# Optimization experiments

Hardware: AMD Instinct MI355X
Metric: run time of the kernel (lower is better)

Reference implementation:

```python
import jax, jax.numpy as jnp
import numpy as np

H = W = 512
MAX_ID = 15          # instance ids 1..15 (0 = background)
N_SIGMA = 1
FG_WEIGHT = 1.0
W_INST, W_VAR, W_SEED = 1.0, 10.0, 1.0


def make_xym(h, w):
    # channel 0 varies along width (x), channel 1 along height (y), like the torch buffer
    xs = jnp.linspace(0.0, 1.0, 512)
    xm = jnp.broadcast_to(xs[None, None, :], (1, 512, 512))
    ym = jnp.broadcast_to(xs[None, :, None], (1, 512, 512))
    xym = jnp.concatenate([xm, ym], axis=0)
    return xym[:, :h, :w]


def lovasz_hinge_flat(logits, labels):
    # logits, labels: flat [P]; labels in {0,1} float
    signs = 2.0 * labels - 1.0
    errors = 1.0 - logits * signs
    perm = jnp.argsort(-errors)                 # descending
    errors_sorted = errors[perm]
    gt_sorted = labels[perm]
    gts = jnp.sum(gt_sorted)
    intersection = gts - jnp.cumsum(gt_sorted)
    union = gts + jnp.cumsum(1.0 - gt_sorted)
    jaccard = 1.0 - intersection / union
    jaccard = jnp.concatenate([jaccard[:1], jaccard[1:] - jaccard[:-1]])
    return jnp.sum(jax.nn.relu(errors_sorted) * jaccard)


def _per_image(pred_b, inst_b, lab_b, xym):
    spatial_emb = jnp.tanh(pred_b[0:2]) + xym          # (2,H,W)
    sigma = pred_b[2]                                  # (H,W), n_sigma=1
    seed_map = jax.nn.sigmoid(pred_b[3])               # (H,W)

    bg = (lab_b == 0)
    seed_bg = jnp.sum(jnp.where(bg, seed_map ** 2, 0.0))

    def per_inst(iid):
        m = (inst_b == iid).astype(pred_b.dtype)       # (H,W)
        cnt = jnp.sum(m)
        present = cnt > 0
        cnt_s = jnp.maximum(cnt, 1.0)
        # to_center=True: center from coordinate map
        center = jnp.sum(xym * m[None], axis=(1, 2)) / cnt_s            # (2,)
        sig_mean = jnp.sum(sigma * m) / cnt_s
        var_l = jnp.sum((sigma - jax.lax.stop_gradient(sig_mean)) ** 2 * m) / cnt_s
        s = jnp.exp(sig_mean * 10.0)
        d2 = jnp.sum((spatial_emb - center[:, None, None]) ** 2, axis=0)  # (H,W)
        dist = jnp.exp(-d2 * s)
        inst_l = lovasz_hinge_flat(dist.reshape(-1) * 2.0 - 1.0, m.reshape(-1))
        seed_l = jnp.sum((seed_map - jax.lax.stop_gradient(dist)) ** 2 * m)
        intra_l = 1.0 - jnp.sum(dist * m) / cnt_s
        return present, var_l, inst_l, seed_l, intra_l

    ids = jnp.arange(1, MAX_ID + 1)
    present, var_l, inst_l, seed_l, intra_l = jax.vmap(per_inst)(ids)
    pf = present.astype(pred_b.dtype)
    obj = jnp.sum(pf)
    obj_s = jnp.maximum(obj, 1.0)
    instance_loss = jnp.sum(inst_l * pf) / obj_s
    var_loss = jnp.sum(var_l * pf) / obj_s
    intra_loss = jnp.sum(intra_l * pf)          # NOT divided by obj_count (as in source)
    seed_loss = (seed_bg + FG_WEIGHT * jnp.sum(seed_l * pf)) / (H * W)
    return W_INST * instance_loss + W_VAR * var_loss + W_SEED * seed_loss + 5.0 * intra_loss


def setup_inputs() -> dict:
    key = jax.random.key(0)
    k1, k2, k3 = jax.random.split(key, 3)
    prediction = jax.random.normal(k1, (4, 4, H, W), dtype=jnp.float32)
    instances = jax.random.randint(k2, (4, H, W), 0, MAX_ID + 1, dtype=jnp.int32)
    labels = jax.random.randint(k3, (4, H, W), 0, 2, dtype=jnp.int32)
    return {"prediction": prediction, "instances": instances, "labels": labels}


def reference(prediction, instances, labels):
    xym = make_xym(prediction.shape[2], prediction.shape[3])
    per_b = jax.vmap(_per_image, in_axes=(0, 0, 0, None))(prediction, instances, labels, xym)
    return jnp.mean(per_b)
```

## Files before the change

### kernel.cpp

```cpp
#include <hip/hip_runtime.h>

#define HW     262144
#define NB     4
#define NID    15
#define KB     256
#define CHUNKS 128
#define PXC    (HW / CHUNKS)

#define WS_TICKET 0
#define WS_GACC   4
#define WS_SBGR   24
#define WS_PART   64
#define PART_STR  1024
#define WS_FACC   65600
#define WS_HIST   90432
#define HIST_U32  (NB * CHUNKS * NID * KB)
#define WS_EMBX   (WS_HIST + HIST_U32)
#define MAP_SZ    (NB * HW)
#define WS_EMBY   (WS_EMBX + MAP_SZ)
#define WS_SEEDM  (WS_EMBY + MAP_SZ)
#define WS_TOTAL  (WS_SEEDM + MAP_SZ)

__device__ __forceinline__ float rcp_fast(float x) { return __builtin_amdgcn_rcpf(x); }
__device__ __forceinline__ float fast_tanh(float x) {
    return 1.0f - 2.0f * rcp_fast(__expf(2.0f * x) + 1.0f);
}
__device__ __forceinline__ float fast_sigmoid(float x) {
    return rcp_fast(1.0f + __expf(-x));
}
__device__ __forceinline__ float atomic_read(float* p) { return atomicAdd(p, 0.0f); }

__global__ __launch_bounds__(256) void prepKernel(const float* __restrict__ pred,
                                                  const int* __restrict__ inst,
                                                  const int* __restrict__ lab,
                                                  float* __restrict__ ws) {
    __shared__ float s_acc[16][68];
    const int b   = blockIdx.y;
    const int tid = threadIdx.x;
    for (int j = tid; j < 16 * 68; j += 256) ((float*)s_acc)[j] = 0.f;
    __syncthreads();

    const int grp = tid >> 4;
    const int ib = b * HW;
    const float* p0 = pred + (((size_t)(b * 4 + 0)) << 18);
    const float* p1 = pred + (((size_t)(b * 4 + 1)) << 18);
    const float* p2 = pred + (((size_t)(b * 4 + 2)) << 18);
    const float* p3 = pred + (((size_t)(b * 4 + 3)) << 18);
    float* embx  = ws + WS_EMBX + ib;
    float* emby  = ws + WS_EMBY + ib;
    float* seedm = ws + WS_SEEDM + ib;
    const float inv511 = 1.0f / 511.0f;

    const int p = blockIdx.x * 1024 + tid * 4;
    const int4   i4 = *(const int4*)(inst + ib + p);
    const int4   l4 = *(const int4*)(lab + ib + p);
    const float4 a4 = *(const float4*)(p0 + p);
    const float4 b4 = *(const float4*)(p1 + p);
    const float4 g4 = *(const float4*)(p2 + p);
    const float4 t4 = *(const float4*)(p3 + p);
    const float xs0 = (float)(p & 511) * inv511;
    const float ys  = (float)(p >> 9) * inv511;

    float4 ex, ey, sd;
    ex.x = fast_tanh(a4.x) + xs0;
    ex.y = fast_tanh(a4.y) + xs0 + inv511;
    ex.z = fast_tanh(a4.z) + xs0 + 2.f * inv511;
    ex.w = fast_tanh(a4.w) + xs0 + 3.f * inv511;
    ey.x = fast_tanh(b4.x) + ys;
    ey.y = fast_tanh(b4.y) + ys;
    ey.z = fast_tanh(b4.z) + ys;
    ey.w = fast_tanh(b4.w) + ys;
    sd.x = fast_sigmoid(t4.x);
    sd.y = fast_sigmoid(t4.y);
    sd.z = fast_sigmoid(t4.z);
    sd.w = fast_sigmoid(t4.w);
    *(float4*)(embx + p)  = ex;
    *(float4*)(emby + p)  = ey;
    *(float4*)(seedm + p) = sd;

    float sbg = 0.f;
    sbg += (l4.x == 0) ? sd.x * sd.x : 0.f;
    sbg += (l4.y == 0) ? sd.y * sd.y : 0.f;
    sbg += (l4.z == 0) ? sd.z * sd.z : 0.f;
    sbg += (l4.w == 0) ? sd.w * sd.w : 0.f;

#define ACC_PX(IID, XS, SG)                                   \
    if ((IID) > 0) {                                          \
        float* a = &s_acc[grp][((IID) - 1) * 4];              \
        atomicAdd(a + 0, 1.f);                                \
        atomicAdd(a + 1, (XS));                               \
        atomicAdd(a + 2, ys);                                 \
        atomicAdd(a + 3, (SG));                               \
    }
    ACC_PX(i4.x, xs0, g4.x)
    ACC_PX(i4.y, xs0 + inv511, g4.y)
    ACC_PX(i4.z, xs0 + 2.f * inv511, g4.z)
    ACC_PX(i4.w, xs0 + 3.f * inv511, g4.w)
#undef ACC_PX

#pragma unroll
    for (int m = 32; m; m >>= 1) sbg += __shfl_xor(sbg, m, 64);
    if ((tid & 63) == 0) atomicAdd(&s_acc[grp][60], sbg);
    __syncthreads();

    if (tid < 61) {
        float tot = 0.f;
#pragma unroll
        for (int q = 0; q < 16; ++q) tot += s_acc[q][tid];
        ws[WS_PART + tid * PART_STR + b * 256 + blockIdx.x] = tot;
    }
    if (blockIdx.x == 0 && b == 0) {
        if (tid < 20)       ws[WS_GACC + tid] = 0.f;
        else if (tid == 20) ((unsigned*)ws)[WS_TICKET] = 0u;
    }
}

#define HCOPY_STRIDE (NID * KB + 1)
__global__ __launch_bounds__(256) void histKernel(const float* __restrict__ pred,
                                                  const int* __restrict__ inst,
                                                  float* __restrict__ ws) {
    __shared__ unsigned s_hist[4 * HCOPY_STRIDE];
    __shared__ float4   s_stat4[NID];
    __shared__ float    s_facc[8][48];
    __shared__ float    s_comp[61];

    const int b     = blockIdx.y;
    const int chunk = blockIdx.x;
    const int tid   = threadIdx.x;
    const int wv = tid >> 6, lane = tid & 63;

    for (int c = wv; c < 61; c += 4) {
        const float* pp = ws + WS_PART + c * PART_STR + b * 256;
        float v = pp[lane] + pp[lane + 64] + pp[lane + 128] + pp[lane + 192];
#pragma unroll
        for (int m = 32; m; m >>= 1) v += __shfl_xor(v, m, 64);
        if (lane == 0) s_comp[c] = v;
    }
    for (int j = tid; j < 4 * HCOPY_STRIDE; j += 256) s_hist[j] = 0u;
    for (int j = tid; j < 8 * 48; j += 256) ((float*)s_facc)[j] = 0.f;
    __syncthreads();

    if (tid < NID) {
        float cnt = s_comp[tid * 4 + 0];
        float ic = rcp_fast(fmaxf(cnt, 1.f));
        float sigm = s_comp[tid * 4 + 3] * ic;
        s_stat4[tid] = make_float4(s_comp[tid * 4 + 1] * ic, s_comp[tid * 4 + 2] * ic,
                                   sigm, __expf(10.f * sigm));
    }
    if (chunk == 0 && tid == 16) ws[WS_SBGR + b] = s_comp[60];
    __syncthreads();

    float csx[NID], csy[NID], css[NID];
#pragma unroll
    for (int i = 0; i < NID; ++i) {
        float4 v = s_stat4[i];
        csx[i] = v.x; csy[i] = v.y; css[i] = v.w;
    }

    unsigned* myhist = &s_hist[((tid >> 4) & 3) * HCOPY_STRIDE];
    float* myfacc = s_facc[(tid >> 3) & 7];
    const int ib = b * HW;
    const float* sig   = pred + (((size_t)(b * 4 + 2)) << 18);
    const float* embx  = ws + WS_EMBX + ib;
    const float* emby  = ws + WS_EMBY + ib;
    const float* seedm = ws + WS_SEEDM + ib;

    auto doPx = [&](float exv, float eyv, float sdv, float gv, int iid) {
#pragma unroll
        for (int i = 0; i < NID; ++i) {
            float dx = exv - csx[i], dy = eyv - csy[i];
            float dist = __expf(-(dx * dx + dy * dy) * css[i]);
            float u1 = dist * (float)KB;
            bool m = (iid == i + 1);
            float bf = m ? ((float)KB - u1) : u1;
            int bk = min((int)bf, KB - 1);
            atomicAdd(&myhist[i * KB + bk], m ? 1u : 0x10000u);
        }
        if (iid > 0) {
            float4 st = s_stat4[iid - 1];
            float dx = exv - st.x, dy = eyv - st.y;
            float dist = __expf(-(dx * dx + dy * dy) * st.w);
            float dsg = gv - st.z;
            float e2 = sdv - dist;
            float* fa = &myfacc[(iid - 1) * 3];
            atomicAdd(fa + 0, dsg * dsg);
            atomicAdd(fa + 1, e2 * e2);
            atomicAdd(fa + 2, dist);
        }
    };

#pragma unroll
    for (int u = 0; u < 2; ++u) {
        const int p = chunk * PXC + u * 1024 + tid * 4;
        const int4   i4 = *(const int4*)(inst + ib + p);
        const float4 exq = *(const float4*)(embx + p);
        const float4 eyq = *(const float4*)(emby + p);
        const float4 sdq = *(const float4*)(seedm + p);
        const float4 gq  = *(const float4*)(sig + p);
        doPx(exq.x, eyq.x, sdq.x, gq.x, i4.x);
        doPx(exq.y, eyq.y, sdq.y, gq.y, i4.y);
        doPx(exq.z, eyq.z, sdq.z, gq.z, i4.z);
        doPx(exq.w, eyq.w, sdq.w, gq.w, i4.w);
    }
    __syncthreads();

    unsigned* dst = (unsigned*)(ws + WS_HIST) + (size_t)(b * CHUNKS + chunk) * (NID * KB);
    for (int j = tid; j < NID * KB; j += 256) {
        dst[j] = s_hist[j] + s_hist[HCOPY_STRIDE + j] +
                 s_hist[2 * HCOPY_STRIDE + j] + s_hist[3 * HCOPY_STRIDE + j];
    }
    if (tid < 45) {
        float tot = 0.f;
#pragma unroll
        for (int q = 0; q < 8; ++q) tot += s_facc[q][tid];
        ws[WS_FACC + (size_t)(b * CHUNKS + chunk) * 48 + tid] = tot;
    }
}

__global__ __launch_bounds__(256) void lovaszKernel(float* __restrict__ ws,
                                                    float* __restrict__ out) {
    __shared__ unsigned s_pf[4][KB];
    __shared__ unsigned s_pb[4][KB];
    __shared__ float s4[4];
    __shared__ float s_f[4][3];
    const int t = blockIdx.x;
    const int b = t / NID, i = t % NID;
    const int tid = threadIdx.x, wv = tid >> 6, lane = tid & 63;

    {
        float g = ws[WS_PART + (i * 4) * PART_STR + b * 256 + tid];
#pragma unroll
        for (int m = 32; m; m >>= 1) g += __shfl_xor(g, m, 64);
        if (lane == 0) s4[wv] = g;
    }
    {
        float f0 = 0.f, f1 = 0.f, f2 = 0.f;
        if (tid < CHUNKS) {
            const float* fb = ws + WS_FACC + (size_t)(b * CHUNKS + tid) * 48 + i * 3;
            f0 = fb[0]; f1 = fb[1]; f2 = fb[2];
        }
#pragma unroll
        for (int m = 32; m; m >>= 1) {
            f0 += __shfl_xor(f0, m, 64);
            f1 += __shfl_xor(f1, m, 64);
            f2 += __shfl_xor(f2, m, 64);
        }
        if (lane == 0) { s_f[wv][0] = f0; s_f[wv][1] = f1; s_f[wv][2] = f2; }
    }
    __syncthreads();
    const float G = s4[0] + s4[1] + s4[2] + s4[3];

    if (G > 0.f) {
        unsigned af0 = 0, af1 = 0, af2 = 0, af3 = 0;
        unsigned ab0 = 0, ab1 = 0, ab2 = 0, ab3 = 0;
        const unsigned* histU = (const unsigned*)(ws + WS_HIST);
        for (int k = 0; k < 32; ++k) {
            const int c = wv * 32 + k;
            const unsigned* hb = histU + ((size_t)(b * CHUNKS + c) * NID + i) * KB + lane * 4;
            uint4 q = *(const uint4*)hb;
            af0 += q.x & 0xffffu; ab0 += q.x >> 16;
            af1 += q.y & 0xffffu; ab1 += q.y >> 16;
            af2 += q.z & 0xffffu; ab2 += q.z >> 16;
            af3 += q.w & 0xffffu; ab3 += q.w >> 16;
        }
        s_pf[wv][lane * 4 + 0] = af0; s_pb[wv][lane * 4 + 0] = ab0;
        s_pf[wv][lane * 4 + 1] = af1; s_pb[wv][lane * 4 + 1] = ab1;
        s_pf[wv][lane * 4 + 2] = af2; s_pb[wv][lane * 4 + 2] = ab2;
        s_pf[wv][lane * 4 + 3] = af3; s_pb[wv][lane * 4 + 3] = ab3;
    }
    __syncthreads();

    float sum = 0.f;
    if (wv == 0 && G > 0.f) {
        float fgs[4], bgs[4];
#pragma unroll
        for (int q = 0; q < 4; ++q) {
            int k = lane * 4 + q;
            fgs[q] = (float)(s_pf[0][k] + s_pf[1][k] + s_pf[2][k] + s_pf[3][k]);
            bgs[q] = (float)(s_pb[0][k] + s_pb[1][k] + s_pb[2][k] + s_pb[3][k]);
        }
        float Fl = fgs[0] + fgs[1] + fgs[2] + fgs[3];
        float Bl = bgs[0] + bgs[1] + bgs[2] + bgs[3];
        float Fs = Fl, Bs = Bl;
#pragma unroll
        for (int d = 1; d < 64; d <<= 1) {
            float fu = __shfl_down(Fs, d, 64);
            float bu = __shfl_down(Bs, d, 64);
            if (lane + d < 64) { Fs += fu; Bs += bu; }
        }
        float F = Fs - Fl, B = Bs - Bl;
        float Jprev = 1.f - (G - F) * rcp_fast(G + B);
        const float ew = 2.f / (float)KB;
#pragma unroll
        for (int q = 3; q >= 0; --q) {
            F += fgs[q]; B += bgs[q];
            float J = 1.f - (G - F) * rcp_fast(G + B);
            float ek = ((float)(lane * 4 + q) + 0.5f) * ew;
            sum += ek * (J - Jprev);
            Jprev = J;
        }
#pragma unroll
        for (int m = 32; m; m >>= 1) sum += __shfl_xor(sum, m, 64);
    }

    if (tid == 0 && G > 0.f) {
        float ic = rcp_fast(fmaxf(G, 1.f));
        float F0 = s_f[0][0] + s_f[1][0] + s_f[2][0] + s_f[3][0];
        float F1 = s_f[0][1] + s_f[1][1] + s_f[2][1] + s_f[3][1];
        float F2 = s_f[0][2] + s_f[1][2] + s_f[2][2] + s_f[3][2];
        float* ga = ws + WS_GACC + b * 5;
        atomicAdd(ga + 0, 1.f);
        atomicAdd(ga + 1, sum);
        atomicAdd(ga + 2, F0 * ic);
        atomicAdd(ga + 3, 1.f - F2 * ic);
        atomicAdd(ga + 4, F1);
    }
    __threadfence();
    if (tid == 0) {
        unsigned tk = atomicAdd((unsigned*)ws + WS_TICKET, 1u);
        if (tk == 59u) {
            float total = 0.f;
            for (int bb = 0; bb < NB; ++bb) {
                float* ga = ws + WS_GACC + bb * 5;
                float obj   = atomic_read(ga + 0);
                float instl = atomic_read(ga + 1);
                float varl  = atomic_read(ga + 2);
                float intral= atomic_read(ga + 3);
                float seedl = atomic_read(ga + 4);
                float sbg   = ws[WS_SBGR + bb];
                float objs  = fmaxf(obj, 1.f);
                total += instl / objs
                       + 10.f * (varl / objs)
                       + (sbg + seedl) / (float)HW
                       + 5.f * intral;
            }
            out[0] = total * 0.25f;
        }
    }
}

extern "C" void kernel_launch(void* const* d_in, const int* in_sizes, int n_in,
                              void* d_out, int out_size, void* d_ws, size_t ws_size,
                              hipStream_t stream) {
    const float* pred = (const float*)d_in[0];
    const int*   inst = (const int*)d_in[1];
    const int*   lab  = (const int*)d_in[2];
    float* ws  = (float*)d_ws;
    float* out = (float*)d_out;

    prepKernel<<<dim3(256, NB), 256, 0, stream>>>(pred, inst, lab, ws);
    histKernel<<<dim3(CHUNKS, NB), 256, 0, stream>>>(pred, inst, ws);
    lovaszKernel<<<60, 256, 0, stream>>>(ws, out);
}
```

Measured before the change: 83.63 us.

## Add stat-reduction kernel, halve histogram bins, reuse matched distance, use exp2

Moves the per-instance centre/sigma reduction out of every histogram block into a small dedicated kernel that writes precomputed stats, so each hist block no longer re-reduces 61 partial arrays. Halves the Lovasz histogram to 128 bins with twice as many chunks, which shrinks per-block shared memory and the per-chunk copy-out, and doubles the number of hist blocks. Folds the bin scale into an exp2 exponent and reuses the matched instance's distance instead of recomputing it. The coarser bins change the Lovasz approximation accuracy, and the extra kernel launch adds some overhead.

```diff
diff --git a/kernel.cpp b/kernel.cpp
--- a/kernel.cpp
+++ b/kernel.cpp
@@ -3,17 +3,19 @@
 #define HW     262144
 #define NB     4
 #define NID    15
-#define KB     256
-#define CHUNKS 128
+#define KB     128
+#define CHUNKS 256
 #define PXC    (HW / CHUNKS)
 
 #define WS_TICKET 0
 #define WS_GACC   4
-#define WS_SBGR   24
-#define WS_PART   64
+#define WS_SBG    24
+#define WS_CNT    28
+#define WS_STAT4  96
+#define WS_PART   512
 #define PART_STR  1024
-#define WS_FACC   65600
-#define WS_HIST   90432
+#define WS_FACC   62976
+#define WS_HIST   112128
 #define HIST_U32  (NB * CHUNKS * NID * KB)
 #define WS_EMBX   (WS_HIST + HIST_U32)
 #define MAP_SZ    (NB * HW)
@@ -21,12 +23,19 @@
 #define WS_SEEDM  (WS_EMBY + MAP_SZ)
 #define WS_TOTAL  (WS_SEEDM + MAP_SZ)
 
+#if __has_builtin(__builtin_amdgcn_exp2f)
+#define EXP2(x) __builtin_amdgcn_exp2f(x)
+#else
+#define EXP2(x) exp2f(x)
+#endif
+#define LOG2E 1.44269504f
+
 __device__ __forceinline__ float rcp_fast(float x) { return __builtin_amdgcn_rcpf(x); }
 __device__ __forceinline__ float fast_tanh(float x) {
-    return 1.0f - 2.0f * rcp_fast(__expf(2.0f * x) + 1.0f);
+    return 1.0f - 2.0f * rcp_fast(EXP2(2.0f * LOG2E * x) + 1.0f);
 }
 __device__ __forceinline__ float fast_sigmoid(float x) {
-    return rcp_fast(1.0f + __expf(-x));
+    return rcp_fast(1.0f + EXP2(-LOG2E * x));
 }
 __device__ __forceinline__ float atomic_read(float* p) { return atomicAdd(p, 0.0f); }
 
@@ -109,9 +118,35 @@
         for (int q = 0; q < 16; ++q) tot += s_acc[q][tid];
         ws[WS_PART + tid * PART_STR + b * 256 + blockIdx.x] = tot;
     }
-    if (blockIdx.x == 0 && b == 0) {
-        if (tid < 20)       ws[WS_GACC + tid] = 0.f;
-        else if (tid == 20) ((unsigned*)ws)[WS_TICKET] = 0u;
+}
+
+__global__ __launch_bounds__(256) void statRedKernel(float* __restrict__ ws) {
+    __shared__ float s_red[61];
+    const int b = blockIdx.x;
+    const int tid = threadIdx.x, wv = tid >> 6, lane = tid & 63;
+
+    for (int c = wv; c < 61; c += 4) {
+        const float* pp = ws + WS_PART + c * PART_STR + b * 256;
+        float v = pp[lane] + pp[lane + 64] + pp[lane + 128] + pp[lane + 192];
+#pragma unroll
+        for (int m = 32; m; m >>= 1) v += __shfl_xor(v, m, 64);
+        if (lane == 0) s_red[c] = v;
+    }
+    __syncthreads();
+
+    if (tid < NID) {
+        float cnt = s_red[tid * 4 + 0];
+        float ic = rcp_fast(fmaxf(cnt, 1.f));
+        float sigm = s_red[tid * 4 + 3] * ic;
+        float sp = EXP2(10.f * LOG2E * sigm) * LOG2E;
+        *(float4*)(ws + WS_STAT4 + (b * NID + tid) * 4) =
+            make_float4(s_red[tid * 4 + 1] * ic, s_red[tid * 4 + 2] * ic, sigm, sp);
+        ws[WS_CNT + b * NID + tid] = cnt;
+    }
+    if (tid == 15) ws[WS_SBG + b] = s_red[60];
+    if (b == 0) {
+        if (tid >= 32 && tid < 52) ws[WS_GACC + tid - 32] = 0.f;
+        if (tid == 52)             ((unsigned*)ws)[WS_TICKET] = 0u;
     }
 }
 
@@ -122,39 +157,21 @@
     __shared__ unsigned s_hist[4 * HCOPY_STRIDE];
     __shared__ float4   s_stat4[NID];
     __shared__ float    s_facc[8][48];
-    __shared__ float    s_comp[61];
 
     const int b     = blockIdx.y;
     const int chunk = blockIdx.x;
     const int tid   = threadIdx.x;
-    const int wv = tid >> 6, lane = tid & 63;
-
-    for (int c = wv; c < 61; c += 4) {
-        const float* pp = ws + WS_PART + c * PART_STR + b * 256;
-        float v = pp[lane] + pp[lane + 64] + pp[lane + 128] + pp[lane + 192];
-#pragma unroll
-        for (int m = 32; m; m >>= 1) v += __shfl_xor(v, m, 64);
-        if (lane == 0) s_comp[c] = v;
-    }
+
+    if (tid < NID) s_stat4[tid] = *(const float4*)(ws + WS_STAT4 + (b * NID + tid) * 4);
     for (int j = tid; j < 4 * HCOPY_STRIDE; j += 256) s_hist[j] = 0u;
     for (int j = tid; j < 8 * 48; j += 256) ((float*)s_facc)[j] = 0.f;
     __syncthreads();
 
-    if (tid < NID) {
-        float cnt = s_comp[tid * 4 + 0];
-        float ic = rcp_fast(fmaxf(cnt, 1.f));
-        float sigm = s_comp[tid * 4 + 3] * ic;
-        s_stat4[tid] = make_float4(s_comp[tid * 4 + 1] * ic, s_comp[tid * 4 + 2] * ic,
-                                   sigm, __expf(10.f * sigm));
-    }
-    if (chunk == 0 && tid == 16) ws[WS_SBGR + b] = s_comp[60];
-    __syncthreads();
-
-    float csx[NID], csy[NID], css[NID];
+    float csx[NID], csy[NID], csp[NID];
 #pragma unroll
     for (int i = 0; i < NID; ++i) {
         float4 v = s_stat4[i];
-        csx[i] = v.x; csy[i] = v.y; css[i] = v.w;
+        csx[i] = v.x; csy[i] = v.y; csp[i] = v.w;
     }
 
     unsigned* myhist = &s_hist[((tid >> 4) & 3) * HCOPY_STRIDE];
@@ -166,21 +183,22 @@
     const float* seedm = ws + WS_SEEDM + ib;
 
     auto doPx = [&](float exv, float eyv, float sdv, float gv, int iid) {
+        float u1m = 0.f;
 #pragma unroll
         for (int i = 0; i < NID; ++i) {
             float dx = exv - csx[i], dy = eyv - csy[i];
-            float dist = __expf(-(dx * dx + dy * dy) * css[i]);
-            float u1 = dist * (float)KB;
+            float d2 = dx * dx + dy * dy;
+            float u1 = EXP2(7.0f - d2 * csp[i]);
             bool m = (iid == i + 1);
+            if (m) u1m = u1;
             float bf = m ? ((float)KB - u1) : u1;
             int bk = min((int)bf, KB - 1);
             atomicAdd(&myhist[i * KB + bk], m ? 1u : 0x10000u);
         }
         if (iid > 0) {
-            float4 st = s_stat4[iid - 1];
-            float dx = exv - st.x, dy = eyv - st.y;
-            float dist = __expf(-(dx * dx + dy * dy) * st.w);
-            float dsg = gv - st.z;
+            float dist = u1m * (1.f / (float)KB);
+            float sigm = s_stat4[iid - 1].z;
+            float dsg = gv - sigm;
             float e2 = sdv - dist;
             float* fa = &myfacc[(iid - 1) * 3];
             atomicAdd(fa + 0, dsg * dsg);
@@ -189,19 +207,16 @@
         }
     };
 
-#pragma unroll
-    for (int u = 0; u < 2; ++u) {
-        const int p = chunk * PXC + u * 1024 + tid * 4;
-        const int4   i4 = *(const int4*)(inst + ib + p);
-        const float4 exq = *(const float4*)(embx + p);
-        const float4 eyq = *(const float4*)(emby + p);
-        const float4 sdq = *(const float4*)(seedm + p);
-        const float4 gq  = *(const float4*)(sig + p);
-        doPx(exq.x, eyq.x, sdq.x, gq.x, i4.x);
-        doPx(exq.y, eyq.y, sdq.y, gq.y, i4.y);
-        doPx(exq.z, eyq.z, sdq.z, gq.z, i4.z);
-        doPx(exq.w, eyq.w, sdq.w, gq.w, i4.w);
-    }
+    const int p = chunk * PXC + tid * 4;
+    const int4   i4 = *(const int4*)(inst + ib + p);
+    const float4 exq = *(const float4*)(embx + p);
+    const float4 eyq = *(const float4*)(emby + p);
+    const float4 sdq = *(const float4*)(seedm + p);
+    const float4 gq  = *(const float4*)(sig + p);
+    doPx(exq.x, eyq.x, sdq.x, gq.x, i4.x);
+    doPx(exq.y, eyq.y, sdq.y, gq.y, i4.y);
+    doPx(exq.z, eyq.z, sdq.z, gq.z, i4.z);
+    doPx(exq.w, eyq.w, sdq.w, gq.w, i4.w);
     __syncthreads();
 
     unsigned* dst = (unsigned*)(ws + WS_HIST) + (size_t)(b * CHUNKS + chunk) * (NID * KB);
@@ -221,24 +236,16 @@
                                                     float* __restrict__ out) {
     __shared__ unsigned s_pf[4][KB];
     __shared__ unsigned s_pb[4][KB];
-    __shared__ float s4[4];
     __shared__ float s_f[4][3];
     const int t = blockIdx.x;
     const int b = t / NID, i = t % NID;
     const int tid = threadIdx.x, wv = tid >> 6, lane = tid & 63;
 
+    const float G = ws[WS_CNT + t];
+
     {
-        float g = ws[WS_PART + (i * 4) * PART_STR + b * 256 + tid];
-#pragma unroll
-        for (int m = 32; m; m >>= 1) g += __shfl_xor(g, m, 64);
-        if (lane == 0) s4[wv] = g;
-    }
-    {
-        float f0 = 0.f, f1 = 0.f, f2 = 0.f;
-        if (tid < CHUNKS) {
-            const float* fb = ws + WS_FACC + (size_t)(b * CHUNKS + tid) * 48 + i * 3;
-            f0 = fb[0]; f1 = fb[1]; f2 = fb[2];
-        }
+        const float* fb = ws + WS_FACC + (size_t)(b * CHUNKS + tid) * 48 + i * 3;
+        float f0 = fb[0], f1 = fb[1], f2 = fb[2];
 #pragma unroll
         for (int m = 32; m; m >>= 1) {
             f0 += __shfl_xor(f0, m, 64);
@@ -247,40 +254,33 @@
         }
         if (lane == 0) { s_f[wv][0] = f0; s_f[wv][1] = f1; s_f[wv][2] = f2; }
     }
-    __syncthreads();
-    const float G = s4[0] + s4[1] + s4[2] + s4[3];
 
     if (G > 0.f) {
-        unsigned af0 = 0, af1 = 0, af2 = 0, af3 = 0;
-        unsigned ab0 = 0, ab1 = 0, ab2 = 0, ab3 = 0;
+        unsigned af0 = 0, af1 = 0, ab0 = 0, ab1 = 0;
         const unsigned* histU = (const unsigned*)(ws + WS_HIST);
-        for (int k = 0; k < 32; ++k) {
-            const int c = wv * 32 + k;
-            const unsigned* hb = histU + ((size_t)(b * CHUNKS + c) * NID + i) * KB + lane * 4;
-            uint4 q = *(const uint4*)hb;
+        for (int k = 0; k < 64; ++k) {
+            const int c = wv * 64 + k;
+            const unsigned* hb = histU + ((size_t)(b * CHUNKS + c) * NID + i) * KB + lane * 2;
+            uint2 q = *(const uint2*)hb;
             af0 += q.x & 0xffffu; ab0 += q.x >> 16;
             af1 += q.y & 0xffffu; ab1 += q.y >> 16;
-            af2 += q.z & 0xffffu; ab2 += q.z >> 16;
-            af3 += q.w & 0xffffu; ab3 += q.w >> 16;
-        }
-        s_pf[wv][lane * 4 + 0] = af0; s_pb[wv][lane * 4 + 0] = ab0;
-        s_pf[wv][lane * 4 + 1] = af1; s_pb[wv][lane * 4 + 1] = ab1;
-        s_pf[wv][lane * 4 + 2] = af2; s_pb[wv][lane * 4 + 2] = ab2;
-        s_pf[wv][lane * 4 + 3] = af3; s_pb[wv][lane * 4 + 3] = ab3;
+        }
+        s_pf[wv][lane * 2 + 0] = af0; s_pb[wv][lane * 2 + 0] = ab0;
+        s_pf[wv][lane * 2 + 1] = af1; s_pb[wv][lane * 2 + 1] = ab1;
     }
     __syncthreads();
 
     float sum = 0.f;
     if (wv == 0 && G > 0.f) {
-        float fgs[4], bgs[4];
-#pragma unroll
-        for (int q = 0; q < 4; ++q) {
-            int k = lane * 4 + q;
+        float fgs[2], bgs[2];
+#pragma unroll
+        for (int q = 0; q < 2; ++q) {
+            int k = lane * 2 + q;
             fgs[q] = (float)(s_pf[0][k] + s_pf[1][k] + s_pf[2][k] + s_pf[3][k]);
             bgs[q] = (float)(s_pb[0][k] + s_pb[1][k] + s_pb[2][k] + s_pb[3][k]);
         }
-        float Fl = fgs[0] + fgs[1] + fgs[2] + fgs[3];
-        float Bl = bgs[0] + bgs[1] + bgs[2] + bgs[3];
+        float Fl = fgs[0] + fgs[1];
+        float Bl = bgs[0] + bgs[1];
         float Fs = Fl, Bs = Bl;
 #pragma unroll
         for (int d = 1; d < 64; d <<= 1) {
@@ -292,10 +292,10 @@
         float Jprev = 1.f - (G - F) * rcp_fast(G + B);
         const float ew = 2.f / (float)KB;
 #pragma unroll
-        for (int q = 3; q >= 0; --q) {
+        for (int q = 1; q >= 0; --q) {
             F += fgs[q]; B += bgs[q];
             float J = 1.f - (G - F) * rcp_fast(G + B);
-            float ek = ((float)(lane * 4 + q) + 0.5f) * ew;
+            float ek = ((float)(lane * 2 + q) + 0.5f) * ew;
             sum += ek * (J - Jprev);
             Jprev = J;
         }
@@ -327,7 +327,7 @@
                 float varl  = atomic_read(ga + 2);
                 float intral= atomic_read(ga + 3);
                 float seedl = atomic_read(ga + 4);
-                float sbg   = ws[WS_SBGR + bb];
+                float sbg   = ws[WS_SBG + bb];
                 float objs  = fmaxf(obj, 1.f);
                 total += instl / objs
                        + 10.f * (varl / objs)
@@ -349,6 +349,7 @@
     float* out = (float*)d_out;
 
     prepKernel<<<dim3(256, NB), 256, 0, stream>>>(pred, inst, lab, ws);
+    statRedKernel<<<NB, 256, 0, stream>>>(ws);
     histKernel<<<dim3(CHUNKS, NB), 256, 0, stream>>>(pred, inst, ws);
     lovaszKernel<<<60, 256, 0, stream>>>(ws, out);
 }
```

After: 82.25 us. No clear change (-1.7%).
